# Kernel optimization log

Hardware: AMD Instinct MI355X
Metric: run time of the kernel (lower is better)

The kernel has to match this reference:

```python
import jax, jax.numpy as jnp
import numpy as np

KERNEL = 3
PAD = KERNEL // 2  # 1


def setup_inputs() -> dict:
    key = jax.random.key(0)
    k1, k2, k3, k4 = jax.random.split(key, 4)
    B, C, H, W = 8, 1, 352, 1216
    affinity = jax.random.normal(k1, (B, KERNEL * KERNEL, H, W), dtype=jnp.float32)
    feature = jax.random.normal(k2, (B, C, H, W), dtype=jnp.float32)
    depth_vals = jax.random.uniform(k3, (B, C, H, W), dtype=jnp.float32, minval=0.1, maxval=80.0)
    valid = (jax.random.uniform(k4, (B, C, H, W), dtype=jnp.float32) < 0.05).astype(jnp.float32)
    sparse_depth = depth_vals * valid
    return {"affinity": affinity, "feature": feature, "sparse_depth": sparse_depth, "times": 24}


def reference(affinity, feature, sparse_depth, times):
    b, k2, h, w = affinity.shape  # k2 == 9
    aff_abs = jnp.abs(affinity)
    aff_norm = aff_abs / jnp.sum(aff_abs, axis=1, keepdims=True)  # [B,9,H,W]
    mask = jnp.sign(sparse_depth)
    feat = (1.0 - mask) * feature + mask * sparse_depth

    def step(f, _):
        fp = jnp.pad(f, ((0, 0), (0, 0), (PAD, PAD), (PAD, PAD)))
        # 9 shifted views, stacked on leading axis: [9, B, C, H, W]
        views = jnp.stack([fp[:, :, i:h + i, j:w + j]
                           for i in range(KERNEL) for j in range(KERNEL)])
        out = jnp.einsum('kbchw,bkhw->bchw', views, aff_norm)
        out = (1.0 - mask) * out + mask * sparse_depth
        return out, None

    feat, _ = jax.lax.scan(step, feat, None, length=times)
    return feat
```

## Files before the change

kernel.cpp:

```cpp
#include <hip/hip_runtime.h>

#define BATCH 8
#define HGT 352
#define WID 1216
#define HW (HGT * WID)
#define NG 304

#define KSTEP 8
#define TGX 16
#define TY  32
#define CGX 20
#define CROWS 46
#define R0GX 22
#define R0ROWS 48
#define LROW 92
#define EROW 21
#define NPAIR 10
#define PSTRIDE 48
#define NTHREADS 512
#define XTILES 19
#define YTILES 11

__global__ __launch_bounds__(256) void weights_kernel(
    const float* __restrict__ aff,
    const float* __restrict__ sparse,
    unsigned short* __restrict__ wout)
{
    const int xg = blockIdx.x * 64 + threadIdx.x;
    const int y  = blockIdx.y * 4 + threadIdx.y;
    const int b  = blockIdx.z;
    if (xg >= NG) return;
    const int x0 = xg * 4;
    const long pix = (long)y * WID + x0;
    const float* ab = aff + (long)b * 9 * HW + pix;

    float4 a[9];
    #pragma unroll
    for (int k = 0; k < 9; ++k)
        a[k] = *(const float4*)(ab + (long)k * HW);
    const float4 sp = *(const float4*)(sparse + (long)b * HW + pix);
    const float m[4] = {sp.x, sp.y, sp.z, sp.w};

    union { uint4 q[4]; unsigned short u[32]; } W;

    #pragma unroll
    for (int p = 0; p < 4; ++p) {
        float av[9], s = 0.0f;
        #pragma unroll
        for (int k = 0; k < 9; ++k) {
            const float* ap = (const float*)&a[k];
            av[k] = fabsf(ap[p]);
            s += av[k];
        }
        const float scale = 65536.0f / s;
        const bool meas = m[p] > 0.0f;
        const int korder[8] = {0, 1, 2, 3, 5, 6, 7, 8};
        #pragma unroll
        for (int ks = 0; ks < 8; ++ks) {
            float t = av[korder[ks]] * scale;
            t = fminf(t, 65535.0f);
            unsigned u = meas ? 0u : (unsigned)t;
            W.u[ks * 4 + p] = (unsigned short)u;
        }
    }

    uint4* dst = (uint4*)wout + ((long)((b * HGT + y) * NG + xg)) * 4;
    dst[0] = W.q[0]; dst[1] = W.q[1]; dst[2] = W.q[2]; dst[3] = W.q[3];
}

__device__ __forceinline__ float4 stencil_g(
    const uint4* wv4, const float* A, const float* B, const float* Cc)
{
    const unsigned* w = (const unsigned*)wv4;
    float acc[4];
    #pragma unroll
    for (int p = 0; p < 4; ++p) {
        unsigned s8 = 0; float ac = 0.0f; unsigned u;
        #define EXW(ks) ((w[((ks) * 4 + p) >> 1] >> ((p & 1) * 16)) & 0xffffu)
        u = EXW(0); s8 += u; ac += (float)u * A[p];
        u = EXW(1); s8 += u; ac += (float)u * A[p + 1];
        u = EXW(2); s8 += u; ac += (float)u * A[p + 2];
        u = EXW(3); s8 += u; ac += (float)u * B[p];
        u = EXW(4); s8 += u; ac += (float)u * B[p + 2];
        u = EXW(5); s8 += u; ac += (float)u * Cc[p];
        u = EXW(6); s8 += u; ac += (float)u * Cc[p + 1];
        u = EXW(7); s8 += u; ac += (float)u * Cc[p + 2];
        #undef EXW
        ac += (float)(65536u - s8) * B[p + 1];
        acc[p] = ac * (1.0f / 65536.0f);
    }
    return make_float4(acc[0], acc[1], acc[2], acc[3]);
}

__device__ __forceinline__ void load_win(
    const float (*fp)[LROW], const float (*ep)[EROW],
    int row, int px, int p, float* V)
{
    const float* r = fp[row];
    const float4 m0 = *(const float4*)&r[px];
    const float4 m1 = *(const float4*)&r[px + 4];
    V[0] = ep[row][p];
    V[1] = m0.x; V[2] = m0.y; V[3] = m0.z; V[4] = m0.w;
    V[5] = m1.x; V[6] = m1.y; V[7] = m1.z; V[8] = m1.w;
    V[9] = ep[row][10 + p];
}

__device__ __forceinline__ void do_step(
    const float (*fp)[LROW], const float (*ep)[EROW],
    float (*fq)[LROW], float (*eq)[EROW],
    const uint4* wv0, const uint4* wv1,
    bool worker, int p, int cy, int px)
{
    __syncthreads();
    if (worker) {
        float W0[10], W1[10], W2[10];
        load_win(fp, ep, cy,     px, p, W0);
        load_win(fp, ep, cy + 1, px, p, W1);
        load_win(fp, ep, cy + 2, px, p, W2);
        const float4 r0 = stencil_g(wv0, W0, W1, W2);
        const float4 r1 = stencil_g(wv1, W0 + 4, W1 + 4, W2 + 4);
        *(float4*)&fq[cy + 1][px]     = r0;
        *(float4*)&fq[cy + 1][px + 4] = r1;
        if (p != 0) eq[cy + 1][10 + p - 1] = r0.x;
        if (p != 9) eq[cy + 1][p + 1]      = r1.w;
    }
}

__global__ __launch_bounds__(NTHREADS, 4) void prop8_kernel(
    const unsigned short* __restrict__ wgt,
    const float* __restrict__ fsrc,
    const float* __restrict__ feature,
    const float* __restrict__ sparse,
    const int first,
    float* __restrict__ fdst)
{
    __shared__ float lfA[R0ROWS][LROW];
    __shared__ float lfB[R0ROWS][LROW];
    __shared__ float leA[R0ROWS][EROW];
    __shared__ float leB[R0ROWS][EROW];

    const int tid = threadIdx.x;
    const int gx0 = blockIdx.x * TGX;
    const int y0  = blockIdx.y * TY;
    const int b   = blockIdx.z;
    const long fbase = (long)b * HW;

    for (int i = tid; i < R0GX * R0ROWS; i += NTHREADS) {
        const int rgx = i % R0GX;
        const int ry  = i / R0GX;
        const int gcx = gx0 - 3 + rgx;
        const int y   = y0 - 8 + ry;
        float4 v = make_float4(0.f, 0.f, 0.f, 0.f);
        if (gcx >= 0 && gcx < NG && y >= 0 && y < HGT) {
            const long pix = fbase + (long)y * WID + gcx * 4;
            if (first) {
                const float4 sp = *(const float4*)(sparse + pix);
                const float4 ft = *(const float4*)(feature + pix);
                v.x = sp.x > 0.f ? sp.x : ft.x;
                v.y = sp.y > 0.f ? sp.y : ft.y;
                v.z = sp.z > 0.f ? sp.z : ft.z;
                v.w = sp.w > 0.f ? sp.w : ft.w;
            } else {
                v = *(const float4*)(fsrc + pix);
            }
        }
        *(float4*)&lfA[ry][rgx * 4] = v;
        if ((rgx & 1) == 0) {
            if (rgx <= 18) leA[ry][rgx >> 1] = v.w;
        } else if (rgx >= 3) {
            leA[ry][10 + ((rgx - 3) >> 1)] = v.x;
        }
    }

    const int pairx = tid / PSTRIDE;
    const int cy    = tid % PSTRIDE;
    const bool worker = (pairx < NPAIR) && (cy < CROWS);

    uint4 wv[2][4];
    #pragma unroll
    for (int g = 0; g < 2; ++g)
        #pragma unroll
        for (int j = 0; j < 4; ++j)
            wv[g][j] = make_uint4(0u, 0u, 0u, 0u);

    if (worker) {
        const int y = y0 - (KSTEP - 1) + cy;
        #pragma unroll
        for (int g = 0; g < 2; ++g) {
            const int gcx = gx0 - 2 + pairx * 2 + g;
            if (gcx >= 0 && gcx < NG && y >= 0 && y < HGT) {
                const uint4* w4 = (const uint4*)wgt + ((long)((b * HGT + y) * NG + gcx)) * 4;
                wv[g][0] = w4[0]; wv[g][1] = w4[1]; wv[g][2] = w4[2]; wv[g][3] = w4[3];
            }
        }
    }

    const int px = 8 * pairx + 4;

    do_step(lfA, leA, lfB, leB, wv[0], wv[1], worker, pairx, cy, px);
    #pragma unroll 1
    for (int t = 0; t < 3; ++t) {
        do_step(lfB, leB, lfA, leA, wv[0], wv[1], worker, pairx, cy, px);
        do_step(lfA, leA, lfB, leB, wv[0], wv[1], worker, pairx, cy, px);
    }

    __syncthreads();
    if (worker && pairx >= 1 && pairx <= 8 && cy >= KSTEP - 1 && cy < KSTEP - 1 + TY) {
        float W0[10], W1[10], W2[10];
        load_win(lfB, leB, cy,     px, pairx, W0);
        load_win(lfB, leB, cy + 1, px, pairx, W1);
        load_win(lfB, leB, cy + 2, px, pairx, W2);
        const float4 r0 = stencil_g(wv[0], W0, W1, W2);
        const float4 r1 = stencil_g(wv[1], W0 + 4, W1 + 4, W2 + 4);
        const int y = y0 + cy - (KSTEP - 1);
        const int gcx = gx0 - 2 + pairx * 2;
        float* dp = fdst + fbase + (long)y * WID + gcx * 4;
        *(float4*)(dp)     = r0;
        *(float4*)(dp + 4) = r1;
    }
}

extern "C" void kernel_launch(void* const* d_in, const int* in_sizes, int n_in,
                              void* d_out, int out_size, void* d_ws, size_t ws_size,
                              hipStream_t stream)
{
    const float* aff     = (const float*)d_in[0];
    const float* feature = (const float*)d_in[1];
    const float* sparse  = (const float*)d_in[2];

    float* out = (float*)d_out;
    unsigned short* wgt = (unsigned short*)d_ws;
    float* imgA = (float*)((char*)d_ws + (size_t)BATCH * HGT * NG * 64);
    float* imgB = imgA + (size_t)BATCH * HW;

    {
        const dim3 blk(64, 4, 1);
        const dim3 grd((NG + 63) / 64, HGT / 4, BATCH);
        weights_kernel<<<grd, blk, 0, stream>>>(aff, sparse, wgt);
    }

    const dim3 grd(XTILES, YTILES, BATCH);
    prop8_kernel<<<grd, NTHREADS, 0, stream>>>(wgt, feature , feature, sparse, 1, imgA);
    prop8_kernel<<<grd, NTHREADS, 0, stream>>>(wgt, imgA, feature, sparse, 0, imgB);
    prop8_kernel<<<grd, NTHREADS, 0, stream>>>(wgt, imgB, feature, sparse, 0, out);
}
```

Baseline: 396.9 us.

## Compute two rows per thread with register reuse and swizzled LDS layout

Each thread now computes two vertically adjacent rows per step and keeps its own rows in registers, so it reads only the row above and the row below from LDS instead of three rows per output row. The block drops from 512 to 256 threads. LDS rows are widened to 96 floats and float4 columns are XOR-swizzled by row to cut bank conflicts. The result is fewer LDS reads per output and fewer threads, at the cost of more registers per thread and lower per-block parallelism.

After: 1.397 ms. +252.0%, slower.

```diff
diff --git a/kernel.cpp b/kernel.cpp
--- a/kernel.cpp
+++ b/kernel.cpp
@@ -9,15 +9,15 @@
 #define KSTEP 8
 #define TGX 16
 #define TY  32
-#define CGX 20
 #define CROWS 46
 #define R0GX 22
 #define R0ROWS 48
-#define LROW 92
+#define LROW 96
 #define EROW 21
 #define NPAIR 10
-#define PSTRIDE 48
-#define NTHREADS 512
+#define NSTRIP 23
+#define KSTRIDE 24
+#define NTHREADS 256
 #define XTILES 19
 #define YTILES 11
 
@@ -66,6 +66,16 @@
 
     uint4* dst = (uint4*)wout + ((long)((b * HGT + y) * NG + xg)) * 4;
     dst[0] = W.q[0]; dst[1] = W.q[1]; dst[2] = W.q[2]; dst[3] = W.q[3];
+}
+
+__device__ __forceinline__ int swz(int row, int cx) {
+    return cx ^ ((row >> 1) & 7);
+}
+__device__ __forceinline__ float4 lds_r4(const float (*fp)[LROW], int row, int cx) {
+    return *(const float4*)&fp[row][swz(row, cx) * 4];
+}
+__device__ __forceinline__ void lds_w4(float (*fp)[LROW], int row, int cx, float4 v) {
+    *(float4*)&fp[row][swz(row, cx) * 4] = v;
 }
 
 __device__ __forceinline__ float4 stencil_g(
@@ -92,41 +102,53 @@
     return make_float4(acc[0], acc[1], acc[2], acc[3]);
 }
 
-__device__ __forceinline__ void load_win(
-    const float (*fp)[LROW], const float (*ep)[EROW],
-    int row, int px, int p, float* V)
-{
-    const float* r = fp[row];
-    const float4 m0 = *(const float4*)&r[px];
-    const float4 m1 = *(const float4*)&r[px + 4];
+__device__ __forceinline__ void loadwin(
+    const float (*fp)[LROW], const float (*ep)[EROW], int row, int p, float* V)
+{
+    const float4 m0 = lds_r4(fp, row, 2 * p + 1);
+    const float4 m1 = lds_r4(fp, row, 2 * p + 2);
     V[0] = ep[row][p];
     V[1] = m0.x; V[2] = m0.y; V[3] = m0.z; V[4] = m0.w;
     V[5] = m1.x; V[6] = m1.y; V[7] = m1.z; V[8] = m1.w;
     V[9] = ep[row][10 + p];
 }
 
-__device__ __forceinline__ void do_step(
+__device__ __forceinline__ void ownwin(
+    const float (*ep)[EROW], int row, int p, float4 a0, float4 a1, float* V)
+{
+    V[0] = ep[row][p];
+    V[1] = a0.x; V[2] = a0.y; V[3] = a0.z; V[4] = a0.w;
+    V[5] = a1.x; V[6] = a1.y; V[7] = a1.z; V[8] = a1.w;
+    V[9] = ep[row][10 + p];
+}
+
+__device__ __forceinline__ void do_step2(
     const float (*fp)[LROW], const float (*ep)[EROW],
     float (*fq)[LROW], float (*eq)[EROW],
-    const uint4* wv0, const uint4* wv1,
-    bool worker, int p, int cy, int px)
-{
+    const uint4 (*wv)[2][4],
+    bool worker, int p, int ra, int rb,
+    float4& oA0, float4& oA1, float4& oB0, float4& oB1)
+{
+    if (worker) {
+        float WT[10], WA[10], WB[10], WC[10];
+        loadwin(fp, ep, ra - 1, p, WT);
+        ownwin(ep, ra, p, oA0, oA1, WA);
+        ownwin(ep, rb, p, oB0, oB1, WB);
+        loadwin(fp, ep, rb + 1, p, WC);
+        const float4 nA0 = stencil_g(wv[0][0], WT, WA, WB);
+        const float4 nA1 = stencil_g(wv[0][1], WT + 4, WA + 4, WB + 4);
+        const float4 nB0 = stencil_g(wv[1][0], WA, WB, WC);
+        const float4 nB1 = stencil_g(wv[1][1], WA + 4, WB + 4, WC + 4);
+        lds_w4(fq, ra, 2 * p + 1, nA0); lds_w4(fq, ra, 2 * p + 2, nA1);
+        lds_w4(fq, rb, 2 * p + 1, nB0); lds_w4(fq, rb, 2 * p + 2, nB1);
+        if (p != 0) { eq[ra][10 + p - 1] = nA0.x; eq[rb][10 + p - 1] = nB0.x; }
+        if (p != 9) { eq[ra][p + 1]      = nA1.w; eq[rb][p + 1]      = nB1.w; }
+        oA0 = nA0; oA1 = nA1; oB0 = nB0; oB1 = nB1;
+    }
     __syncthreads();
-    if (worker) {
-        float W0[10], W1[10], W2[10];
-        load_win(fp, ep, cy,     px, p, W0);
-        load_win(fp, ep, cy + 1, px, p, W1);
-        load_win(fp, ep, cy + 2, px, p, W2);
-        const float4 r0 = stencil_g(wv0, W0, W1, W2);
-        const float4 r1 = stencil_g(wv1, W0 + 4, W1 + 4, W2 + 4);
-        *(float4*)&fq[cy + 1][px]     = r0;
-        *(float4*)&fq[cy + 1][px + 4] = r1;
-        if (p != 0) eq[cy + 1][10 + p - 1] = r0.x;
-        if (p != 9) eq[cy + 1][p + 1]      = r1.w;
-    }
-}
-
-__global__ __launch_bounds__(NTHREADS, 4) void prop8_kernel(
+}
+
+__global__ __launch_bounds__(NTHREADS, 3) void prop8_kernel(
     const unsigned short* __restrict__ wgt,
     const float* __restrict__ fsrc,
     const float* __restrict__ feature,
@@ -164,7 +186,7 @@
                 v = *(const float4*)(fsrc + pix);
             }
         }
-        *(float4*)&lfA[ry][rgx * 4] = v;
+        lds_w4(lfA, ry, rgx, v);
         if ((rgx & 1) == 0) {
             if (rgx <= 18) leA[ry][rgx >> 1] = v.w;
         } else if (rgx >= 3) {
@@ -172,51 +194,74 @@
         }
     }
 
-    const int pairx = tid / PSTRIDE;
-    const int cy    = tid % PSTRIDE;
-    const bool worker = (pairx < NPAIR) && (cy < CROWS);
-
-    uint4 wv[2][4];
-    #pragma unroll
-    for (int g = 0; g < 2; ++g)
-        #pragma unroll
-        for (int j = 0; j < 4; ++j)
-            wv[g][j] = make_uint4(0u, 0u, 0u, 0u);
+    const int p = tid / KSTRIDE;
+    const int k = tid % KSTRIDE;
+    const bool worker = (p < NPAIR) && (k < NSTRIP);
+    const int ra = 2 * k + 1;
+    const int rb = 2 * k + 2;
+
+    uint4 wv[2][2][4];
+    #pragma unroll
+    for (int r = 0; r < 2; ++r)
+        #pragma unroll
+        for (int g = 0; g < 2; ++g)
+            #pragma unroll
+            for (int j = 0; j < 4; ++j)
+                wv[r][g][j] = make_uint4(0u, 0u, 0u, 0u);
 
     if (worker) {
-        const int y = y0 - (KSTEP - 1) + cy;
-        #pragma unroll
-        for (int g = 0; g < 2; ++g) {
-            const int gcx = gx0 - 2 + pairx * 2 + g;
-            if (gcx >= 0 && gcx < NG && y >= 0 && y < HGT) {
-                const uint4* w4 = (const uint4*)wgt + ((long)((b * HGT + y) * NG + gcx)) * 4;
-                wv[g][0] = w4[0]; wv[g][1] = w4[1]; wv[g][2] = w4[2]; wv[g][3] = w4[3];
+        #pragma unroll
+        for (int r = 0; r < 2; ++r) {
+            const int y = y0 - 8 + (r == 0 ? ra : rb);
+            #pragma unroll
+            for (int g = 0; g < 2; ++g) {
+                const int gcx = gx0 - 2 + p * 2 + g;
+                if (gcx >= 0 && gcx < NG && y >= 0 && y < HGT) {
+                    const uint4* w4 = (const uint4*)wgt + ((long)((b * HGT + y) * NG + gcx)) * 4;
+                    wv[r][g][0] = w4[0]; wv[r][g][1] = w4[1];
+                    wv[r][g][2] = w4[2]; wv[r][g][3] = w4[3];
+                }
             }
         }
     }
 
-    const int px = 8 * pairx + 4;
-
-    do_step(lfA, leA, lfB, leB, wv[0], wv[1], worker, pairx, cy, px);
+    __syncthreads();
+
+    float4 oA0, oA1, oB0, oB1;
+    oA0 = oA1 = oB0 = oB1 = make_float4(0.f, 0.f, 0.f, 0.f);
+    if (worker) {
+        oA0 = lds_r4(lfA, ra, 2 * p + 1); oA1 = lds_r4(lfA, ra, 2 * p + 2);
+        oB0 = lds_r4(lfA, rb, 2 * p + 1); oB1 = lds_r4(lfA, rb, 2 * p + 2);
+    }
+
+    do_step2(lfA, leA, lfB, leB, wv, worker, p, ra, rb, oA0, oA1, oB0, oB1);
     #pragma unroll 1
     for (int t = 0; t < 3; ++t) {
-        do_step(lfB, leB, lfA, leA, wv[0], wv[1], worker, pairx, cy, px);
-        do_step(lfA, leA, lfB, leB, wv[0], wv[1], worker, pairx, cy, px);
-    }
-
-    __syncthreads();
-    if (worker && pairx >= 1 && pairx <= 8 && cy >= KSTEP - 1 && cy < KSTEP - 1 + TY) {
-        float W0[10], W1[10], W2[10];
-        load_win(lfB, leB, cy,     px, pairx, W0);
-        load_win(lfB, leB, cy + 1, px, pairx, W1);
-        load_win(lfB, leB, cy + 2, px, pairx, W2);
-        const float4 r0 = stencil_g(wv[0], W0, W1, W2);
-        const float4 r1 = stencil_g(wv[1], W0 + 4, W1 + 4, W2 + 4);
-        const int y = y0 + cy - (KSTEP - 1);
-        const int gcx = gx0 - 2 + pairx * 2;
-        float* dp = fdst + fbase + (long)y * WID + gcx * 4;
-        *(float4*)(dp)     = r0;
-        *(float4*)(dp + 4) = r1;
+        do_step2(lfB, leB, lfA, leA, wv, worker, p, ra, rb, oA0, oA1, oB0, oB1);
+        do_step2(lfA, leA, lfB, leB, wv, worker, p, ra, rb, oA0, oA1, oB0, oB1);
+    }
+
+    if (worker && p >= 1 && p <= 8) {
+        float WT[10], WA[10], WB[10], WC[10];
+        loadwin(lfB, leB, ra - 1, p, WT);
+        ownwin(leB, ra, p, oA0, oA1, WA);
+        ownwin(leB, rb, p, oB0, oB1, WB);
+        loadwin(lfB, leB, rb + 1, p, WC);
+        const int gcx = gx0 - 2 + p * 2;
+        if (ra >= KSTEP && ra < KSTEP + TY) {
+            const float4 r0 = stencil_g(wv[0][0], WT, WA, WB);
+            const float4 r1 = stencil_g(wv[0][1], WT + 4, WA + 4, WB + 4);
+            float* dp = fdst + fbase + (long)(y0 + ra - KSTEP) * WID + gcx * 4;
+            *(float4*)(dp)     = r0;
+            *(float4*)(dp + 4) = r1;
+        }
+        if (rb >= KSTEP && rb < KSTEP + TY) {
+            const float4 r0 = stencil_g(wv[1][0], WA, WB, WC);
+            const float4 r1 = stencil_g(wv[1][1], WA + 4, WB + 4, WC + 4);
+            float* dp = fdst + fbase + (long)(y0 + rb - KSTEP) * WID + gcx * 4;
+            *(float4*)(dp)     = r0;
+            *(float4*)(dp + 4) = r1;
+        }
     }
 }
 
```
